# Performance work log

Hardware: AMD Instinct MI355X
Metric: run time of the kernel (lower is better)

## Reference

```python
import jax, jax.numpy as jnp
import numpy as np

Q = 3  # q_order: SelfONN concatenates powers x^1..x^Q on channel dim

def selfonn_conv(x, w, b, pad):
    # x: (B, C, H, W); w: (O, C*Q, kh, kw); b: (O,)
    xp = jnp.concatenate([x ** (i + 1) for i in range(Q)], axis=1)
    y = jax.lax.conv_general_dilated(
        xp, w, window_strides=(1, 1), padding=[(pad, pad), (pad, pad)],
        dimension_numbers=("NCHW", "OIHW", "NCHW"))
    return y + b[None, :, None, None]

def setup_inputs() -> dict:
    key = jax.random.key(0)
    ks = jax.random.split(key, 9)
    B, C, H, W = 4, 64, 64, 64
    P = 64  # pab_channels
    s1 = 1.0 / np.sqrt(C * Q)          # 1x1 convs
    s3 = 1.0 / np.sqrt(C * Q * 9)      # 3x3 convs
    return {
        "x": jax.random.normal(ks[0], (B, C, H, W), jnp.float32),
        "top_w": jax.random.normal(ks[1], (P, C * Q, 1, 1), jnp.float32) * s1,
        "top_b": jnp.zeros((P,), jnp.float32),
        "center_w": jax.random.normal(ks[2], (P, C * Q, 1, 1), jnp.float32) * s1,
        "center_b": jnp.zeros((P,), jnp.float32),
        "bottom_w": jax.random.normal(ks[3], (C, C * Q, 3, 3), jnp.float32) * s3,
        "bottom_b": jnp.zeros((C,), jnp.float32),
        "out_w": jax.random.normal(ks[4], (C, C * Q, 3, 3), jnp.float32) * s3,
        "out_b": jnp.zeros((C,), jnp.float32),
    }

def reference(x, top_w, top_b, center_w, center_b, bottom_w, bottom_b, out_w, out_b):
    B, C, H, W = x.shape
    HW = H * W
    x_top = selfonn_conv(x, top_w, top_b, 0).reshape(B, -1, HW)            # (B, P, HW)
    x_center = selfonn_conv(x, center_w, center_b, 0).reshape(B, -1, HW)  # (B, P, HW)
    x_bottom = selfonn_conv(x, bottom_w, bottom_b, 1).reshape(B, C, HW)   # (B, C, HW)
    x_center = jnp.swapaxes(x_center, 1, 2)  # (B, HW, P)
    x_bottom = jnp.swapaxes(x_bottom, 1, 2)  # (B, HW, C)
    sp = jnp.einsum("bnp,bpm->bnm", x_center, x_top)  # (B, HW, HW)
    # GLOBAL softmax over the entire HW*HW map per sample (dim=1 on flattened view)
    sp = jax.nn.softmax(sp.reshape(B, -1), axis=1).reshape(B, HW, HW)
    sp = jnp.einsum("bnm,bmc->bnc", sp, x_bottom)  # (B, HW, C)
    # faithful to torch: raw reshape (B, HW, C) -> (B, C, H, W), no transpose
    sp = sp.reshape(B, C, H, W)
    return selfonn_conv(x + sp, out_w, out_b, 1)
```

## Files before the change

kernel.cpp:

```cpp
#include <hip/hip_runtime.h>
#include <hip/hip_bf16.h>

namespace {
constexpr int IMG    = 262144;
constexpr int MS     = 4;
constexpr int PADIMG = 4356;
constexpr float LOG2E = 1.44269504088896340736f;
constexpr int WBFO  = 0;
constexpr int XPADO = 122880;
constexpr int TOPO  = 1795584;
constexpr int CENO  = 2319872;
constexpr int BOTO  = 2844160;
constexpr int PVO   = 3368448;
constexpr int MSO   = 5465600;
constexpr int ZSO   = 5469696;
}

using half8v  = __attribute__((ext_vector_type(8))) _Float16;
using half4v  = __attribute__((ext_vector_type(4))) _Float16;
using short8v = __attribute__((ext_vector_type(8))) short;
typedef __attribute__((ext_vector_type(4))) float f32x4;

__device__ __forceinline__ short f2bf(float f) {
    __hip_bfloat16 h = __float2bfloat16(f);
    return *reinterpret_cast<short*>(&h);
}
__device__ __forceinline__ float bf2f(short s) {
    unsigned u = ((unsigned)(unsigned short)s) << 16;
    return __uint_as_float(u);
}

__global__ __launch_bounds__(256) void k_prep(const float* __restrict__ bw, const float* __restrict__ ow,
                                              const float* __restrict__ tw, const float* __restrict__ cw,
                                              _Float16* __restrict__ wbf,
                                              const float* __restrict__ x, _Float16* __restrict__ xpad) {
    __shared__ float xs[64 * 65];
    int bx = blockIdx.x, t = threadIdx.x;
    if (bx < 960) {
        int idx = bx * 256 + t;
        if (idx < 221184) {
            int tsel = idx / 110592;
            int r    = idx - tsel * 110592;
            int tap  = r / 12288;
            int rr   = r - tap * 12288;
            int ck   = rr / 2048;
            int r2   = rr - ck * 2048;
            int o    = r2 >> 5;
            int ki   = r2 & 31;
            int k    = ck * 32 + ki;
            int p    = k >> 6, ci = k & 63;
            const float* src = tsel ? ow : bw;
            wbf[idx] = (_Float16)src[o * 1728 + (p * 64 + ci) * 9 + tap];
        } else {
            int j = idx - 221184;
            int tsel = j / 12288;
            int rr   = j - tsel * 12288;
            int ck   = rr / 2048;
            int r2   = rr - ck * 2048;
            int o    = r2 >> 5;
            int ki   = r2 & 31;
            int k    = ck * 32 + ki;
            wbf[idx] = (_Float16)(tsel ? cw[o * 192 + k] * LOG2E : tw[o * 192 + k]);
        }
        return;
    }
    int bx2 = bx - 960;
    int b = bx2 >> 6, h = bx2 & 63;
    {
        _Float16* base = xpad + (size_t)b * 6 * PADIMG * 32;
        int px[6];
        px[0] = (h + 1) * 66;
        px[1] = (h + 1) * 66 + 65;
        px[2] = h;
        px[3] = 65 * 66 + h;
        int npx = 4;
        if (h < 2) { px[4] = 64 + h; px[5] = 65 * 66 + 64 + h; npx = 6; }
        int pi = t / 24, ck = t % 24;
        if (pi < npx) {
            int cp = ck >> 2, q = ck & 3;
            half8v z = {0, 0, 0, 0, 0, 0, 0, 0};
            *(half8v*)&base[((size_t)cp * PADIMG + px[pi]) * 32 + q * 8] = z;
        }
    }
    #pragma unroll
    for (int it = 0; it < 16; ++it) {
        int idx = it * 256 + t;
        int ci = idx >> 6, wc = idx & 63;
        xs[ci * 65 + wc] = x[b * IMG + ci * 4096 + h * 64 + wc];
    }
    __syncthreads();
    _Float16* dst = xpad + ((size_t)b * 6 * PADIMG + (h + 1) * 66 + 1) * 32;
    #pragma unroll
    for (int it = 0; it < 6; ++it) {
        int u = it * 256 + t;
        int ck = u >> 8, within = u & 255;
        int px = within >> 2, q = within & 3;
        int k0 = ck * 32 + q * 8;
        int p = k0 >> 6, c0 = k0 & 63;
        half8v o;
        #pragma unroll
        for (int j = 0; j < 8; ++j) {
            float v = xs[(c0 + j) * 65 + px];
            float pw = (p == 0) ? v : ((p == 1) ? v * v : v * v * v);
            o[j] = (_Float16)pw;
        }
        *(half8v*)&dst[((size_t)ck * PADIMG + px) * 32 + q * 8] = o;
    }
}

__device__ __forceinline__ void conv3d32(int bx, int t,
                                         const _Float16* __restrict__ src,
                                         const _Float16* __restrict__ wt,
                                         const float* __restrict__ bias,
                                         _Float16* __restrict__ dh_, float* __restrict__ df) {
    int lane = t & 63, w = t >> 6;
    int l16 = lane & 15, quad = lane >> 4;
    int oh = bx >> 8, mt = bx & 255;
    int b = mt >> 6, h = mt & 63;
    const _Float16* abase = src + ((size_t)b * 6 * PADIMG + (h + 1) * 66 + 1 + w * 16 + l16) * 32 + quad * 8;
    const _Float16* bbase = wt + (size_t)(oh * 32 + l16) * 32 + quad * 8;
    f32x4 acc[2];
    acc[0] = (f32x4){0.f, 0.f, 0.f, 0.f};
    acc[1] = (f32x4){0.f, 0.f, 0.f, 0.f};
    for (int tap = 0; tap < 9; ++tap) {
        int dh = tap / 3 - 1, dw = tap % 3 - 1;
        const _Float16* arow = abase + (dh * 66 + dw) * 32;
        const _Float16* brow = bbase + (size_t)tap * 6 * 2048;
        #pragma unroll
        for (int c6 = 0; c6 < 6; ++c6) {
            half8v afr  = *(const half8v*)&arow[(size_t)c6 * PADIMG * 32];
            half8v bfr0 = *(const half8v*)&brow[(size_t)c6 * 2048];
            half8v bfr1 = *(const half8v*)&brow[(size_t)c6 * 2048 + 512];
            acc[0] = __builtin_amdgcn_mfma_f32_16x16x32_f16(afr, bfr0, acc[0], 0, 0, 0);
            acc[1] = __builtin_amdgcn_mfma_f32_16x16x32_f16(afr, bfr1, acc[1], 0, 0, 0);
        }
    }
    #pragma unroll
    for (int nf = 0; nf < 2; ++nf) {
        int c = oh * 32 + nf * 16 + l16;
        float bv = bias[c];
        size_t oi = (size_t)b * 262144 + (size_t)c * 4096 + h * 64 + w * 16 + quad * 4;
        if (dh_) {
            half4v o;
            #pragma unroll
            for (int r = 0; r < 4; ++r) o[r] = (_Float16)(acc[nf][r] + bv);
            *(half4v*)&dh_[oi] = o;
        } else {
            float4 o = make_float4(acc[nf][0] + bv, acc[nf][1] + bv, acc[nf][2] + bv, acc[nf][3] + bv);
            *(float4*)&df[oi] = o;
        }
    }
}

__global__ __launch_bounds__(256) void k_convs(const _Float16* __restrict__ xpad,
                                               const _Float16* __restrict__ wbf,
                                               const float* __restrict__ tb, const float* __restrict__ cb,
                                               const float* __restrict__ bbias,
                                               _Float16* __restrict__ topd, _Float16* __restrict__ cend,
                                               _Float16* __restrict__ botb) {
    int bx = blockIdx.x, t = threadIdx.x;
    if (bx < 512) {
        conv3d32(bx, t, xpad, wbf , bbias, botb, nullptr);
        return;
    }
    int bx2 = bx - 512;
    int lane = t & 63, w = t >> 6;
    int l16 = lane & 15, quad = lane >> 4;
    int ot = bx2 >> 8, mt = bx2 & 255;
    int b = mt >> 6, h = mt & 63;
    const _Float16* wt   = wbf + (ot ? 233472 : 221184);
    const float*    bias = ot ? cb : tb;
    _Float16*       dst  = (ot ? cend : topd) + (size_t)b * IMG;
    const _Float16* abase = xpad + ((size_t)b * 6 * PADIMG + (h + 1) * 66 + 1 + w * 16 + l16) * 32 + quad * 8;
    const _Float16* bbase = wt + (size_t)l16 * 32 + quad * 8;
    f32x4 acc[4];
    #pragma unroll
    for (int nf = 0; nf < 4; ++nf) acc[nf] = (f32x4){0.f, 0.f, 0.f, 0.f};
    #pragma unroll
    for (int kc = 0; kc < 6; ++kc) {
        half8v afr = *(const half8v*)&abase[(size_t)kc * PADIMG * 32];
        #pragma unroll
        for (int nf = 0; nf < 4; ++nf) {
            half8v bfr = *(const half8v*)&bbase[(size_t)kc * 2048 + nf * 16 * 32];
            acc[nf] = __builtin_amdgcn_mfma_f32_16x16x32_f16(afr, bfr, acc[nf], 0, 0, 0);
        }
    }
    _Float16* dp = dst + (size_t)(h * 64 + w * 16) * 64;
    #pragma unroll
    for (int nf = 0; nf < 4; ++nf) {
        float bv = bias[nf * 16 + l16];
        if (ot) bv *= LOG2E;
        #pragma unroll
        for (int r = 0; r < 4; ++r)
            dp[(quad * 4 + r) * 64 + nf * 16 + l16] = (_Float16)(acc[nf][r] + bv);
    }
}

__global__ __launch_bounds__(256, 4) void k_attn(float* __restrict__ ws) {
    __shared__ _Float16 ltop[64 * 72];
    __shared__ _Float16 lbot[64 * 72];
    __shared__ _Float16 lp[64 * 72];
    int t    = threadIdx.x;
    int lane = t & 63, w = t >> 6;
    int l16  = lane & 15, quad = lane >> 4;
    int bx = blockIdx.x;
    int st = bx & 63, b = (bx >> 6) & 3, s = bx >> 8;
    int n0 = st * 64;
    const _Float16* topg = (const _Float16*)(ws + TOPO) + (size_t)b * IMG;
    const _Float16* ceng = (const _Float16*)(ws + CENO) + (size_t)b * IMG;
    const _Float16* botg = (const _Float16*)(ws + BOTO) + (size_t)b * IMG;

    half8v afr[2];
    #pragma unroll
    for (int kk = 0; kk < 2; ++kk)
        afr[kk] = *(const half8v*)&ceng[(size_t)(n0 + w * 16 + l16) * 64 + kk * 32 + quad * 8];

    int r0 = t >> 3, r1 = r0 + 32, off = (t & 7) * 8;
    int q2 = quad >> 1;
    int lpw = (w * 16 + quad * 4) * 72;
    int lpr = (w * 16 + l16) * 72;
    int rb3 = (l16 >> 3) & 1;

    f32x4 pv[4];
    #pragma unroll
    for (int j = 0; j < 4; ++j) pv[j] = (f32x4){0.f, 0.f, 0.f, 0.f};
    float runm = -3.0e38f, zacc = 0.f;

    int mp = s * 1024;
    half8v rt0 = *(const half8v*)&topg[(size_t)(mp + r0) * 64 + off];
    half8v rt1 = *(const half8v*)&topg[(size_t)(mp + r1) * 64 + off];
    half8v rb0 = *(const half8v*)&botg[(size_t)r0 * 4096 + mp + off];
    half8v rb1 = *(const half8v*)&botg[(size_t)r1 * 4096 + mp + off];

    for (int tt = 0; tt < 16; ++tt) {
        __syncthreads();
        *(half8v*)&ltop[r0 * 72 + off] = rt0;
        *(half8v*)&ltop[r1 * 72 + off] = rt1;
        *(half8v*)&lbot[r0 * 72 + off] = rb0;
        *(half8v*)&lbot[r1 * 72 + off] = rb1;
        __syncthreads();
        if (tt < 15) {
            int m1 = s * 1024 + (tt + 1) * 64;
            rt0 = *(const half8v*)&topg[(size_t)(m1 + r0) * 64 + off];
            rt1 = *(const half8v*)&topg[(size_t)(m1 + r1) * 64 + off];
            rb0 = *(const half8v*)&botg[(size_t)r0 * 4096 + m1 + off];
            rb1 = *(const half8v*)&botg[(size_t)r1 * 4096 + m1 + off];
        }
        f32x4 sa[4];
        #pragma unroll
        for (int j = 0; j < 4; ++j) sa[j] = (f32x4){0.f, 0.f, 0.f, 0.f};
        #pragma unroll
        for (int kk = 0; kk < 2; ++kk)
            #pragma unroll
            for (int j = 0; j < 4; ++j) {
                half8v bfr = *(half8v*)&ltop[(j * 16 + l16) * 72 + kk * 32 + quad * 8];
                sa[j] = __builtin_amdgcn_mfma_f32_16x16x32_f16(afr[kk], bfr, sa[j], 0, 0, 0);
            }
        float tm = -3.0e38f;
        #pragma unroll
        for (int j = 0; j < 4; ++j)
            #pragma unroll
            for (int r = 0; r < 4; ++r) tm = fmaxf(tm, sa[j][r]);
        for (int o2 = 32; o2; o2 >>= 1) tm = fmaxf(tm, __shfl_xor(tm, o2, 64));
        float newm = fmaxf(runm, tm);
        if (newm > runm) {
            float sc = exp2f(runm - newm);
            zacc *= sc;
            #pragma unroll
            for (int j = 0; j < 4; ++j) pv[j] *= sc;
            runm = newm;
        }
        #pragma unroll
        for (int j = 0; j < 4; ++j) {
            int cb = (j ^ q2) * 16 + l16;
            #pragma unroll
            for (int r = 0; r < 4; ++r) {
                float e = exp2f(sa[j][r] - runm);
                zacc += e;
                lp[lpw + r * 72 + cb] = (_Float16)e;
            }
        }
        half8v pa[2];
        #pragma unroll
        for (int kk = 0; kk < 2; ++kk) {
            int jj = kk * 2 + q2;
            pa[kk] = *(half8v*)&lp[lpr + ((jj ^ rb3) * 16) + (quad & 1) * 8];
        }
        #pragma unroll
        for (int kk = 0; kk < 2; ++kk)
            #pragma unroll
            for (int j = 0; j < 4; ++j) {
                half8v bb = *(half8v*)&lbot[(j * 16 + l16) * 72 + kk * 32 + quad * 8];
                pv[j] = __builtin_amdgcn_mfma_f32_16x16x32_f16(pa[kk], bb, pv[j], 0, 0, 0);
            }
    }
    for (int o2 = 32; o2; o2 >>= 1) zacc += __shfl_xor(zacc, o2, 64);
    if (lane == 0) {
        ws[MSO + s * 1024 + b * 256 + st * 4 + w] = runm;
        ws[ZSO + s * 1024 + b * 256 + st * 4 + w] = zacc;
    }
    short* pvp = (short*)(ws + PVO) + (size_t)s * 1048576 + (size_t)b * IMG;
    #pragma unroll
    for (int j = 0; j < 4; ++j)
        #pragma unroll
        for (int r = 0; r < 4; ++r)
            pvp[(size_t)(n0 + w * 16 + quad * 4 + r) * 64 + j * 16 + l16] = f2bf(pv[j][r]);
}

__global__ __launch_bounds__(256) void k_finalu(const float* __restrict__ x, float* __restrict__ ws,
                                                _Float16* __restrict__ upad) {
    __shared__ float us[64 * 65];
    __shared__ float rm[4], rz[4];
    int t = threadIdx.x, bx = blockIdx.x;
    int b = bx >> 6, h = bx & 63;
    float mv[4];
    float m = -3.0e38f;
    #pragma unroll
    for (int s = 0; s < 4; ++s) {
        mv[s] = ws[MSO + s * 1024 + b * 256 + t];
        m = fmaxf(m, mv[s]);
    }
    for (int o2 = 32; o2; o2 >>= 1) m = fmaxf(m, __shfl_xor(m, o2, 64));
    if ((t & 63) == 0) rm[t >> 6] = m;
    __syncthreads();
    float M = fmaxf(fmaxf(rm[0], rm[1]), fmaxf(rm[2], rm[3]));
    float z = 0.f;
    #pragma unroll
    for (int s = 0; s < 4; ++s)
        z += ws[ZSO + s * 1024 + b * 256 + t] * exp2f(mv[s] - M);
    for (int o2 = 32; o2; o2 >>= 1) z += __shfl_xor(z, o2, 64);
    if ((t & 63) == 0) rz[t >> 6] = z;
    __syncthreads();
    float Z = rz[0] + rz[1] + rz[2] + rz[3];

    const short* pvb = (const short*)(ws + PVO) + (size_t)b * IMG;
    int hg = h >> 4;
    #pragma unroll
    for (int it = 0; it < 2; ++it) {
        int idx = it * 2048 + t * 8;
        int ci = idx >> 6, wc = idx & 63;
        int rem = ci * 4096 + h * 64 + wc;
        int grp = ci * 4 + hg;
        float acc[8] = {};
        #pragma unroll
        for (int s = 0; s < MS; ++s) {
            float scl = exp2f(ws[MSO + s * 1024 + b * 256 + grp] - M);
            short8v pvv = *(const short8v*)&pvb[(size_t)s * 1048576 + rem];
            #pragma unroll
            for (int i = 0; i < 8; ++i) acc[i] += bf2f(pvv[i]) * scl;
        }
        float4 x0 = *(const float4*)&x[(size_t)b * IMG + rem];
        float4 x1 = *(const float4*)&x[(size_t)b * IMG + rem + 4];
        float xv[8] = {x0.x, x0.y, x0.z, x0.w, x1.x, x1.y, x1.z, x1.w};
        #pragma unroll
        for (int i = 0; i < 8; ++i)
            us[ci * 65 + wc + i] = xv[i] + acc[i] / Z;
    }
    __syncthreads();
    _Float16* dst = upad + ((size_t)b * 6 * PADIMG + (h + 1) * 66 + 1) * 32;
    #pragma unroll
    for (int it = 0; it < 6; ++it) {
        int u = it * 256 + t;
        int ck = u >> 8, within = u & 255;
        int px = within >> 2, q = within & 3;
        int k0 = ck * 32 + q * 8;
        int p = k0 >> 6, c0 = k0 & 63;
        half8v o;
        #pragma unroll
        for (int j = 0; j < 8; ++j) {
            float v = us[(c0 + j) * 65 + px];
            float pw = (p == 0) ? v : ((p == 1) ? v * v : v * v * v);
            o[j] = (_Float16)pw;
        }
        *(half8v*)&dst[((size_t)ck * PADIMG + px) * 32 + q * 8] = o;
    }
}

__global__ __launch_bounds__(256) void k_conv3o(const _Float16* __restrict__ upad,
                                                const _Float16* __restrict__ wout,
                                                const float* __restrict__ ob,
                                                float* __restrict__ out) {
    conv3d32(blockIdx.x, threadIdx.x, upad, wout, ob, nullptr, out);
}

extern "C" void kernel_launch(void* const* d_in, const int* in_sizes, int n_in,
                              void* d_out, int out_size, void* d_ws, size_t ws_size,
                              hipStream_t stream) {
    (void)in_sizes; (void)n_in; (void)out_size; (void)ws_size;
    const float* x  = (const float*)d_in[0];
    const float* tw = (const float*)d_in[1];
    const float* tb = (const float*)d_in[2];
    const float* cw = (const float*)d_in[3];
    const float* cb = (const float*)d_in[4];
    const float* bw = (const float*)d_in[5];
    const float* bb = (const float*)d_in[6];
    const float* ow = (const float*)d_in[7];
    const float* ob = (const float*)d_in[8];
    float* ws  = (float*)d_ws;
    float* out = (float*)d_out;

    _Float16* wbf  = (_Float16*)(ws + WBFO);
    _Float16* wout = wbf + 110592;
    _Float16* xpad = (_Float16*)(ws + XPADO);
    _Float16* topb = (_Float16*)(ws + TOPO);
    _Float16* cenb = (_Float16*)(ws + CENO);
    _Float16* botb = (_Float16*)(ws + BOTO);

    hipLaunchKernelGGL(k_prep, dim3(1216), dim3(256), 0, stream, bw, ow, tw, cw, wbf, x, xpad);
    hipLaunchKernelGGL(k_convs, dim3(1024), dim3(256), 0, stream, xpad, wbf, tb, cb, bb, topb, cenb, botb);
    hipLaunchKernelGGL(k_attn, dim3(1024), dim3(256), 0, stream, ws);
    hipLaunchKernelGGL(k_finalu, dim3(256), dim3(256), 0, stream, x, ws, xpad);
    hipLaunchKernelGGL(k_conv3o, dim3(512), dim3(256), 0, stream, xpad, wout, ob, out);
}
```

Before: 167.4 us.

## Double attention query tile per block to reuse staged top/bottom tiles

Each attention block now handles 128 query rows (32 per wave, two 16-row MFMA fragments) instead of 64, halving the grid to 512 blocks. Every staged tile of top/bottom keys in LDS now feeds twice as many MFMAs, which cuts global and LDS traffic per unit of work. The per-group max/sum buffers shrink, and the finalize kernel's indexing is updated to match. The cost is higher register and LDS use, the dropped occupancy hint in launch bounds, and fewer blocks to fill the CUs.

```diff
diff --git a/kernel.cpp b/kernel.cpp
--- a/kernel.cpp
+++ b/kernel.cpp
@@ -13,7 +13,7 @@
 constexpr int BOTO  = 2844160;
 constexpr int PVO   = 3368448;
 constexpr int MSO   = 5465600;
-constexpr int ZSO   = 5469696;
+constexpr int ZSO   = 5467648;
 }
 
 using half8v  = __attribute__((ext_vector_type(8))) _Float16;
@@ -196,34 +196,38 @@
     }
 }
 
-__global__ __launch_bounds__(256, 4) void k_attn(float* __restrict__ ws) {
+__global__ __launch_bounds__(256) void k_attn(float* __restrict__ ws) {
     __shared__ _Float16 ltop[64 * 72];
     __shared__ _Float16 lbot[64 * 72];
-    __shared__ _Float16 lp[64 * 72];
+    __shared__ _Float16 lp[128 * 72];
     int t    = threadIdx.x;
     int lane = t & 63, w = t >> 6;
     int l16  = lane & 15, quad = lane >> 4;
     int bx = blockIdx.x;
-    int st = bx & 63, b = (bx >> 6) & 3, s = bx >> 8;
-    int n0 = st * 64;
+    int st = bx & 31, b = (bx >> 5) & 3, s = bx >> 7;
+    int n0 = st * 128;
     const _Float16* topg = (const _Float16*)(ws + TOPO) + (size_t)b * IMG;
     const _Float16* ceng = (const _Float16*)(ws + CENO) + (size_t)b * IMG;
     const _Float16* botg = (const _Float16*)(ws + BOTO) + (size_t)b * IMG;
 
-    half8v afr[2];
-    #pragma unroll
-    for (int kk = 0; kk < 2; ++kk)
-        afr[kk] = *(const half8v*)&ceng[(size_t)(n0 + w * 16 + l16) * 64 + kk * 32 + quad * 8];
+    half8v afr[2][2];
+    #pragma unroll
+    for (int i = 0; i < 2; ++i)
+        #pragma unroll
+        for (int kk = 0; kk < 2; ++kk)
+            afr[i][kk] = *(const half8v*)&ceng[(size_t)(n0 + w * 32 + i * 16 + l16) * 64 + kk * 32 + quad * 8];
 
     int r0 = t >> 3, r1 = r0 + 32, off = (t & 7) * 8;
     int q2 = quad >> 1;
-    int lpw = (w * 16 + quad * 4) * 72;
-    int lpr = (w * 16 + l16) * 72;
+    int lpw = (w * 32 + quad * 4) * 72;
+    int lpr = (w * 32 + l16) * 72;
     int rb3 = (l16 >> 3) & 1;
 
-    f32x4 pv[4];
-    #pragma unroll
-    for (int j = 0; j < 4; ++j) pv[j] = (f32x4){0.f, 0.f, 0.f, 0.f};
+    f32x4 pv[2][4];
+    #pragma unroll
+    for (int i = 0; i < 2; ++i)
+        #pragma unroll
+        for (int j = 0; j < 4; ++j) pv[i][j] = (f32x4){0.f, 0.f, 0.f, 0.f};
     float runm = -3.0e38f, zacc = 0.f;
 
     int mp = s * 1024;
@@ -246,65 +250,79 @@
             rb0 = *(const half8v*)&botg[(size_t)r0 * 4096 + m1 + off];
             rb1 = *(const half8v*)&botg[(size_t)r1 * 4096 + m1 + off];
         }
-        f32x4 sa[4];
-        #pragma unroll
-        for (int j = 0; j < 4; ++j) sa[j] = (f32x4){0.f, 0.f, 0.f, 0.f};
+        f32x4 sa[2][4];
+        #pragma unroll
+        for (int i = 0; i < 2; ++i)
+            #pragma unroll
+            for (int j = 0; j < 4; ++j) sa[i][j] = (f32x4){0.f, 0.f, 0.f, 0.f};
         #pragma unroll
         for (int kk = 0; kk < 2; ++kk)
             #pragma unroll
             for (int j = 0; j < 4; ++j) {
                 half8v bfr = *(half8v*)&ltop[(j * 16 + l16) * 72 + kk * 32 + quad * 8];
-                sa[j] = __builtin_amdgcn_mfma_f32_16x16x32_f16(afr[kk], bfr, sa[j], 0, 0, 0);
+                sa[0][j] = __builtin_amdgcn_mfma_f32_16x16x32_f16(afr[0][kk], bfr, sa[0][j], 0, 0, 0);
+                sa[1][j] = __builtin_amdgcn_mfma_f32_16x16x32_f16(afr[1][kk], bfr, sa[1][j], 0, 0, 0);
             }
         float tm = -3.0e38f;
         #pragma unroll
-        for (int j = 0; j < 4; ++j)
-            #pragma unroll
-            for (int r = 0; r < 4; ++r) tm = fmaxf(tm, sa[j][r]);
+        for (int i = 0; i < 2; ++i)
+            #pragma unroll
+            for (int j = 0; j < 4; ++j)
+                #pragma unroll
+                for (int r = 0; r < 4; ++r) tm = fmaxf(tm, sa[i][j][r]);
         for (int o2 = 32; o2; o2 >>= 1) tm = fmaxf(tm, __shfl_xor(tm, o2, 64));
         float newm = fmaxf(runm, tm);
         if (newm > runm) {
             float sc = exp2f(runm - newm);
             zacc *= sc;
             #pragma unroll
-            for (int j = 0; j < 4; ++j) pv[j] *= sc;
+            for (int i = 0; i < 2; ++i)
+                #pragma unroll
+                for (int j = 0; j < 4; ++j) pv[i][j] *= sc;
             runm = newm;
         }
         #pragma unroll
-        for (int j = 0; j < 4; ++j) {
-            int cb = (j ^ q2) * 16 + l16;
-            #pragma unroll
-            for (int r = 0; r < 4; ++r) {
-                float e = exp2f(sa[j][r] - runm);
-                zacc += e;
-                lp[lpw + r * 72 + cb] = (_Float16)e;
+        for (int i = 0; i < 2; ++i)
+            #pragma unroll
+            for (int j = 0; j < 4; ++j) {
+                int cb = (j ^ q2) * 16 + l16;
+                #pragma unroll
+                for (int r = 0; r < 4; ++r) {
+                    float e = exp2f(sa[i][j][r] - runm);
+                    zacc += e;
+                    lp[lpw + i * 1152 + r * 72 + cb] = (_Float16)e;
+                }
             }
-        }
-        half8v pa[2];
-        #pragma unroll
-        for (int kk = 0; kk < 2; ++kk) {
-            int jj = kk * 2 + q2;
-            pa[kk] = *(half8v*)&lp[lpr + ((jj ^ rb3) * 16) + (quad & 1) * 8];
-        }
+        half8v pa[2][2];
+        #pragma unroll
+        for (int i = 0; i < 2; ++i)
+            #pragma unroll
+            for (int kk = 0; kk < 2; ++kk) {
+                int jj = kk * 2 + q2;
+                pa[i][kk] = *(half8v*)&lp[lpr + i * 1152 + ((jj ^ rb3) * 16) + (quad & 1) * 8];
+            }
         #pragma unroll
         for (int kk = 0; kk < 2; ++kk)
             #pragma unroll
             for (int j = 0; j < 4; ++j) {
                 half8v bb = *(half8v*)&lbot[(j * 16 + l16) * 72 + kk * 32 + quad * 8];
-                pv[j] = __builtin_amdgcn_mfma_f32_16x16x32_f16(pa[kk], bb, pv[j], 0, 0, 0);
+                pv[0][j] = __builtin_amdgcn_mfma_f32_16x16x32_f16(pa[0][kk], bb, pv[0][j], 0, 0, 0);
+                pv[1][j] = __builtin_amdgcn_mfma_f32_16x16x32_f16(pa[1][kk], bb, pv[1][j], 0, 0, 0);
             }
     }
     for (int o2 = 32; o2; o2 >>= 1) zacc += __shfl_xor(zacc, o2, 64);
     if (lane == 0) {
-        ws[MSO + s * 1024 + b * 256 + st * 4 + w] = runm;
-        ws[ZSO + s * 1024 + b * 256 + st * 4 + w] = zacc;
+        ws[MSO + s * 512 + b * 128 + st * 4 + w] = runm;
+        ws[ZSO + s * 512 + b * 128 + st * 4 + w] = zacc;
     }
     short* pvp = (short*)(ws + PVO) + (size_t)s * 1048576 + (size_t)b * IMG;
     #pragma unroll
-    for (int j = 0; j < 4; ++j)
-        #pragma unroll
-        for (int r = 0; r < 4; ++r)
-            pvp[(size_t)(n0 + w * 16 + quad * 4 + r) * 64 + j * 16 + l16] = f2bf(pv[j][r]);
+    for (int i = 0; i < 2; ++i)
+        #pragma unroll
+        for (int j = 0; j < 4; ++j)
+            #pragma unroll
+            for (int r = 0; r < 4; ++r)
+                pvp[(size_t)(n0 + w * 32 + i * 16 + quad * 4 + r) * 64 + j * 16 + l16] = f2bf(pv[i][j][r]);
 }
 
 __global__ __launch_bounds__(256) void k_finalu(const float* __restrict__ x, float* __restrict__ ws,
@@ -313,11 +331,12 @@
     __shared__ float rm[4], rz[4];
     int t = threadIdx.x, bx = blockIdx.x;
     int b = bx >> 6, h = bx & 63;
+    int g = t & 127;
     float mv[4];
     float m = -3.0e38f;
     #pragma unroll
     for (int s = 0; s < 4; ++s) {
-        mv[s] = ws[MSO + s * 1024 + b * 256 + t];
+        mv[s] = ws[MSO + s * 512 + b * 128 + g];
         m = fmaxf(m, mv[s]);
     }
     for (int o2 = 32; o2; o2 >>= 1) m = fmaxf(m, __shfl_xor(m, o2, 64));
@@ -325,26 +344,28 @@
     __syncthreads();
     float M = fmaxf(fmaxf(rm[0], rm[1]), fmaxf(rm[2], rm[3]));
     float z = 0.f;
-    #pragma unroll
-    for (int s = 0; s < 4; ++s)
-        z += ws[ZSO + s * 1024 + b * 256 + t] * exp2f(mv[s] - M);
+    if (t < 128) {
+        #pragma unroll
+        for (int s = 0; s < 4; ++s)
+            z += ws[ZSO + s * 512 + b * 128 + g] * exp2f(mv[s] - M);
+    }
     for (int o2 = 32; o2; o2 >>= 1) z += __shfl_xor(z, o2, 64);
     if ((t & 63) == 0) rz[t >> 6] = z;
     __syncthreads();
     float Z = rz[0] + rz[1] + rz[2] + rz[3];
 
     const short* pvb = (const short*)(ws + PVO) + (size_t)b * IMG;
-    int hg = h >> 4;
+    int hg = h >> 5;
     #pragma unroll
     for (int it = 0; it < 2; ++it) {
         int idx = it * 2048 + t * 8;
         int ci = idx >> 6, wc = idx & 63;
         int rem = ci * 4096 + h * 64 + wc;
-        int grp = ci * 4 + hg;
+        int grp = ci * 2 + hg;
         float acc[8] = {};
         #pragma unroll
         for (int s = 0; s < MS; ++s) {
-            float scl = exp2f(ws[MSO + s * 1024 + b * 256 + grp] - M);
+            float scl = exp2f(ws[MSO + s * 512 + b * 128 + grp] - M);
             short8v pvv = *(const short8v*)&pvb[(size_t)s * 1048576 + rem];
             #pragma unroll
             for (int i = 0; i < 8; ++i) acc[i] += bf2f(pvv[i]) * scl;
@@ -408,7 +429,7 @@
 
     hipLaunchKernelGGL(k_prep, dim3(1216), dim3(256), 0, stream, bw, ow, tw, cw, wbf, x, xpad);
     hipLaunchKernelGGL(k_convs, dim3(1024), dim3(256), 0, stream, xpad, wbf, tb, cb, bb, topb, cenb, botb);
-    hipLaunchKernelGGL(k_attn, dim3(1024), dim3(256), 0, stream, ws);
+    hipLaunchKernelGGL(k_attn, dim3(512), dim3(256), 0, stream, ws);
     hipLaunchKernelGGL(k_finalu, dim3(256), dim3(256), 0, stream, x, ws, xpad);
     hipLaunchKernelGGL(k_conv3o, dim3(512), dim3(256), 0, stream, xpad, wout, ob, out);
 }
```

New measurement: 165.9 us. No clear change (-0.9%).
